# Performance work log

Measured on AMD Instinct MI355X. Metric: run time of the kernel, lower is better.

## Reference

```python
import jax, jax.numpy as jnp
import numpy as np

SHIFT = 1  # fixed instance of the random +/-1 shift_direction


def setup_inputs() -> dict:
    key = jax.random.key(0)
    k1, k2 = jax.random.split(key)
    x = jax.random.normal(k1, (128, 256, 28, 28), dtype=jnp.float32)
    W = jax.random.normal(k2, (128, 3, 128), dtype=jnp.float32)  # (j=in, k=3, i=out)
    return {"x": x, "W": W}


def reference(x, W):
    B, G, Cg, H, Wd = 128, 2, 128, 28, 28
    # view as (l, o, j, n, m) = (batch, group, chan, h, w)
    xg = x.reshape(B, G, Cg, H, Wd)
    # circular roll along width (original: roll(t, shift, dim=4))
    xg = jnp.roll(xg, SHIFT, axis=4)
    # unfold(3,1) pad (1,0) + einsum 'lojnmk, jki -> lonmi' is exactly a
    # zero-padded 1D conv along width with full channel mixing, shared over
    # group and h. Express it as a single grouped-batch conv.
    xm = xg.reshape(B * G, Cg, H, Wd)                 # (N, C, H, W)
    kern = jnp.transpose(W, (2, 0, 1))[:, :, None, :]  # (i, j, 1, 3) OIHW
    y = jax.lax.conv_general_dilated(
        xm, kern, window_strides=(1, 1), padding=((0, 0), (1, 1)),
        dimension_numbers=("NCHW", "OIHW", "NCHW"))   # (B*G, i, H, W)
    y = y.reshape(B, G, Cg, H, Wd)                    # (l, o, i, n, m)
    # second roll is along h (dim 1 of the (l,n,m,o*i) layout == n here)
    y = jnp.roll(y, SHIFT, axis=3)
    # final layout (l, o*i, n, m) == (128, 256, 28, 28)
    return y.reshape(B, G * Cg, H, Wd)
```

## Files before the change

kernel.cpp:

```cpp
#include <hip/hip_runtime.h>


typedef __bf16 bf16x8 __attribute__((ext_vector_type(8)));
typedef float  f32x4  __attribute__((ext_vector_type(4)));

__device__ __forceinline__ int swz(int r, int j) {
    return r * 128 + (j ^ ((r & 7) << 3));
}

#define STAGE_WRITE(BUF, V, J, MQ)                                   \
    {                                                                \
        _Pragma("unroll")                                            \
        for (int e = 0; e < 4; ++e) {                                \
            const int m = (MQ) * 4 + e;                              \
            const int r = (m == 27) ? 1 : (m + 2);                   \
            union { __bf16 h; unsigned short u; } cv;                \
            cv.h = (__bf16)((&(V).x)[e]);                            \
            xsp[BUF][swz(r, (J))] = cv.u;                            \
        }                                                            \
    }

__global__ __launch_bounds__(512, 4)
void shiftconv_kernel(const float* __restrict__ x,
                      const float* __restrict__ Wm,
                      float* __restrict__ out)
{
    __shared__ unsigned short xsp[2][34 * 128];

    const int tid  = threadIdx.x;
    const int wave = tid >> 6;
    const int lane = tid & 63;
    const int l15  = lane & 15;
    const int hi2  = lane >> 4;

    const int b  = blockIdx.x;
    const int l  = b >> 3;
    const int o  = (b >> 2) & 1;
    const int nc = b & 3;

    const float* xbase = x   + (size_t)(l * 256 + o * 128) * 784;
    float*       obase = out + (size_t)(l * 256 + o * 128) * 784;

    const int ga  = tid;
    const int gb  = tid + 512;
    const int ja  = ga / 7,  ma = ga - ja * 7;
    const int jb2 = gb / 7,  mb = gb - jb2 * 7;
    const bool vb = (gb < 896);

    int n1 = nc * 7;

    float4 pa = *reinterpret_cast<const float4*>(xbase + ja * 784 + n1 * 28 + ma * 4);
    float4 pb = make_float4(0.f, 0.f, 0.f, 0.f);
    if (vb) pb = *reinterpret_cast<const float4*>(xbase + jb2 * 784 + n1 * 28 + mb * 4);

    const int ig = wave * 16 + l15;
    bf16x8 bw[12];
#pragma unroll
    for (int s = 0; s < 12; ++s) {
        const int kw = s >> 2;
        const int jb = (s & 3) * 32 + hi2 * 8;
#pragma unroll
        for (int e = 0; e < 8; ++e)
            bw[s][e] = (__bf16)Wm[((jb + e) * 3 + kw) * 128 + ig];
    }

    {
        const int buf = tid >> 8;
        const int r   = ((tid >> 7) & 1) ? 29 : 0;
        const int j   = tid & 127;
        xsp[buf][swz(r, j)] = 0;
    }

    STAGE_WRITE(0, pa, ja, ma);
    if (vb) STAGE_WRITE(0, pb, jb2, mb);

    int cur = 0;
#pragma unroll 1
    for (int t = 0; t < 7; ++t) {
        __syncthreads();

        float4 na, nb;
        const bool more = (t < 6);
        if (more) {
            na = *reinterpret_cast<const float4*>(xbase + ja * 784 + (n1 + 1) * 28 + ma * 4);
            if (vb) nb = *reinterpret_cast<const float4*>(xbase + jb2 * 784 + (n1 + 1) * 28 + mb * 4);
        }

        f32x4 acc0 = {0.f, 0.f, 0.f, 0.f};
        f32x4 acc1 = {0.f, 0.f, 0.f, 0.f};
        const unsigned short* xs = xsp[cur];
#pragma unroll
        for (int s = 0; s < 12; ++s) {
            const int kw = s >> 2;
            const int jb = (s & 3) * 32 + hi2 * 8;
            const bf16x8 a0 = *reinterpret_cast<const bf16x8*>(&xs[swz(l15 + kw, jb)]);
            acc0 = __builtin_amdgcn_mfma_f32_16x16x32_bf16(a0, bw[s], acc0, 0, 0, 0);
            const bf16x8 a1 = *reinterpret_cast<const bf16x8*>(&xs[swz(16 + l15 + kw, jb)]);
            acc1 = __builtin_amdgcn_mfma_f32_16x16x32_bf16(a1, bw[s], acc1, 0, 0, 0);
        }

        const int n = (n1 + 1) % 28;
        float* op = obase + (size_t)ig * 784 + n * 28;
        *reinterpret_cast<float4*>(op + hi2 * 4) =
            make_float4(acc0[0], acc0[1], acc0[2], acc0[3]);
        if (hi2 < 3)
            *reinterpret_cast<float4*>(op + 16 + hi2 * 4) =
                make_float4(acc1[0], acc1[1], acc1[2], acc1[3]);

        if (more) {
            STAGE_WRITE(cur ^ 1, na, ja, ma);
            if (vb) STAGE_WRITE(cur ^ 1, nb, jb2, mb);
        }
        cur ^= 1;
        ++n1;
    }
}

extern "C" void kernel_launch(void* const* d_in, const int* in_sizes, int n_in,
                              void* d_out, int out_size, void* d_ws, size_t ws_size,
                              hipStream_t stream) {
    const float* x  = (const float*)d_in[0];
    const float* Wm = (const float*)d_in[1];
    float* out = (float*)d_out;
    hipLaunchKernelGGL(shiftconv_kernel, dim3(1024), dim3(512), 0, stream, x, Wm, out);
}
```

Before: 222.7 us.

## Split output channels across blocks and prefetch input rows two ahead

Halves the block size to 256 threads and doubles the grid, so each block computes 64 output channels instead of 128. Input rows are now loaded two iterations ahead into register sets, and the loop is fully unrolled with raw s_barrier calls and s_setprio around the MFMA section. The LDS swizzle is also changed to key on row pairs. The cost is that each block stages the full input rows for only half the outputs, so input reads and bf16 conversions are duplicated across the two channel halves.

```diff
diff --git a/kernel.cpp b/kernel.cpp
--- a/kernel.cpp
+++ b/kernel.cpp
@@ -5,22 +5,35 @@
 typedef float  f32x4  __attribute__((ext_vector_type(4)));
 
 __device__ __forceinline__ int swz(int r, int j) {
-    return r * 128 + (j ^ ((r & 7) << 3));
+    return r * 128 + (j ^ (((r >> 1) & 7) << 3));
 }
 
-#define STAGE_WRITE(BUF, V, J, MQ)                                   \
-    {                                                                \
-        _Pragma("unroll")                                            \
-        for (int e = 0; e < 4; ++e) {                                \
-            const int m = (MQ) * 4 + e;                              \
-            const int r = (m == 27) ? 1 : (m + 2);                   \
-            union { __bf16 h; unsigned short u; } cv;                \
-            cv.h = (__bf16)((&(V).x)[e]);                            \
-            xsp[BUF][swz(r, (J))] = cv.u;                            \
-        }                                                            \
+#define LOADROW(SET, T)                                                        \
+    {                                                                          \
+        SET[0] = *reinterpret_cast<const float4*>(cbase[0] + (T) * 28);        \
+        SET[1] = *reinterpret_cast<const float4*>(cbase[1] + (T) * 28);        \
+        SET[2] = *reinterpret_cast<const float4*>(cbase[2] + (T) * 28);        \
+        if (v3) SET[3] = *reinterpret_cast<const float4*>(cbase[3] + (T) * 28);\
     }
 
-__global__ __launch_bounds__(512, 4)
+#define STAGEROW(SET, BUF)                                                     \
+    {                                                                          \
+        _Pragma("unroll")                                                      \
+        for (int c = 0; c < 4; ++c) {                                          \
+            if (c < 3 || v3) {                                                 \
+                _Pragma("unroll")                                              \
+                for (int e = 0; e < 4; ++e) {                                  \
+                    const int m = cm[c] * 4 + e;                               \
+                    const int r = (m == 27) ? 1 : (m + 2);                     \
+                    union { __bf16 h; unsigned short u; } cv;                  \
+                    cv.h = (__bf16)((&SET[c].x)[e]);                           \
+                    xsp[BUF][swz(r, cj[c])] = cv.u;                            \
+                }                                                              \
+            }                                                                  \
+        }                                                                      \
+    }
+
+__global__ __launch_bounds__(256, 4)
 void shiftconv_kernel(const float* __restrict__ x,
                       const float* __restrict__ Wm,
                       float* __restrict__ out)
@@ -34,26 +47,16 @@
     const int hi2  = lane >> 4;
 
     const int b  = blockIdx.x;
-    const int l  = b >> 3;
-    const int o  = (b >> 2) & 1;
+    const int l  = b >> 4;
+    const int o  = (b >> 3) & 1;
+    const int ih = (b >> 2) & 1;
     const int nc = b & 3;
 
-    const float* xbase = x   + (size_t)(l * 256 + o * 128) * 784;
+    const float* xbase = x   + (size_t)(l * 256 + o * 128) * 784 + nc * 7 * 28;
     float*       obase = out + (size_t)(l * 256 + o * 128) * 784;
 
-    const int ga  = tid;
-    const int gb  = tid + 512;
-    const int ja  = ga / 7,  ma = ga - ja * 7;
-    const int jb2 = gb / 7,  mb = gb - jb2 * 7;
-    const bool vb = (gb < 896);
+    const int ig = ih * 64 + wave * 16 + l15;
 
-    int n1 = nc * 7;
-
-    float4 pa = *reinterpret_cast<const float4*>(xbase + ja * 784 + n1 * 28 + ma * 4);
-    float4 pb = make_float4(0.f, 0.f, 0.f, 0.f);
-    if (vb) pb = *reinterpret_cast<const float4*>(xbase + jb2 * 784 + n1 * 28 + mb * 4);
-
-    const int ig = wave * 16 + l15;
     bf16x8 bw[12];
 #pragma unroll
     for (int s = 0; s < 12; ++s) {
@@ -64,31 +67,48 @@
             bw[s][e] = (__bf16)Wm[((jb + e) * 3 + kw) * 128 + ig];
     }
 
-    {
-        const int buf = tid >> 8;
-        const int r   = ((tid >> 7) & 1) ? 29 : 0;
-        const int j   = tid & 127;
-        xsp[buf][swz(r, j)] = 0;
+    int cj[4], cm[4];
+    const float* cbase[4];
+#pragma unroll
+    for (int c = 0; c < 4; ++c) {
+        const int g = tid + 256 * c;
+        const int j = g / 7;
+        cj[c] = j;
+        cm[c] = g - j * 7;
+        cbase[c] = xbase + j * 784 + cm[c] * 4;
+    }
+    const bool v3 = (tid < 128);
+
+#pragma unroll
+    for (int k = 0; k < 2; ++k) {
+        const int idx = tid + 256 * k;
+        const int bu  = idx >> 8;
+        const int r   = (idx & 128) ? 29 : 0;
+        const int j   = idx & 127;
+        xsp[bu][swz(r, j)] = 0;
     }
 
-    STAGE_WRITE(0, pa, ja, ma);
-    if (vb) STAGE_WRITE(0, pb, jb2, mb);
+    float4 ra[4], rb[4];
+    LOADROW(ra, 0);
+    LOADROW(rb, 1);
+    STAGEROW(ra, 0);
+    asm volatile("s_waitcnt lgkmcnt(0)" ::: "memory");
+    __builtin_amdgcn_sched_barrier(0);
+    __builtin_amdgcn_s_barrier();
+    __builtin_amdgcn_sched_barrier(0);
 
-    int cur = 0;
-#pragma unroll 1
+#pragma unroll
     for (int t = 0; t < 7; ++t) {
-        __syncthreads();
+        const int cur = t & 1;
 
-        float4 na, nb;
-        const bool more = (t < 6);
-        if (more) {
-            na = *reinterpret_cast<const float4*>(xbase + ja * 784 + (n1 + 1) * 28 + ma * 4);
-            if (vb) nb = *reinterpret_cast<const float4*>(xbase + jb2 * 784 + (n1 + 1) * 28 + mb * 4);
+        if (t + 2 < 7) {
+            if (cur == 0) { LOADROW(ra, t + 2) } else { LOADROW(rb, t + 2) }
         }
 
         f32x4 acc0 = {0.f, 0.f, 0.f, 0.f};
         f32x4 acc1 = {0.f, 0.f, 0.f, 0.f};
         const unsigned short* xs = xsp[cur];
+        __builtin_amdgcn_s_setprio(1);
 #pragma unroll
         for (int s = 0; s < 12; ++s) {
             const int kw = s >> 2;
@@ -98,8 +118,10 @@
             const bf16x8 a1 = *reinterpret_cast<const bf16x8*>(&xs[swz(16 + l15 + kw, jb)]);
             acc1 = __builtin_amdgcn_mfma_f32_16x16x32_bf16(a1, bw[s], acc1, 0, 0, 0);
         }
+        __builtin_amdgcn_s_setprio(0);
 
-        const int n = (n1 + 1) % 28;
+        const int n1 = nc * 7 + t;
+        int n = n1 + 1; if (n == 28) n = 0;
         float* op = obase + (size_t)ig * 784 + n * 28;
         *reinterpret_cast<float4*>(op + hi2 * 4) =
             make_float4(acc0[0], acc0[1], acc0[2], acc0[3]);
@@ -107,12 +129,13 @@
             *reinterpret_cast<float4*>(op + 16 + hi2 * 4) =
                 make_float4(acc1[0], acc1[1], acc1[2], acc1[3]);
 
-        if (more) {
-            STAGE_WRITE(cur ^ 1, na, ja, ma);
-            if (vb) STAGE_WRITE(cur ^ 1, nb, jb2, mb);
+        if (t + 1 < 7) {
+            if (cur == 0) { STAGEROW(rb, 1) } else { STAGEROW(ra, 0) }
+            asm volatile("s_waitcnt lgkmcnt(0)" ::: "memory");
+            __builtin_amdgcn_sched_barrier(0);
+            __builtin_amdgcn_s_barrier();
+            __builtin_amdgcn_sched_barrier(0);
         }
-        cur ^= 1;
-        ++n1;
     }
 }
 
@@ -122,5 +145,5 @@
     const float* x  = (const float*)d_in[0];
     const float* Wm = (const float*)d_in[1];
     float* out = (float*)d_out;
-    hipLaunchKernelGGL(shiftconv_kernel, dim3(1024), dim3(512), 0, stream, x, Wm, out);
+    hipLaunchKernelGGL(shiftconv_kernel, dim3(2048), dim3(256), 0, stream, x, Wm, out);
 }
```

Measured after the change: 384.0 us. 1.72x slower.

## Preload all seven rows into LDS with one sync and transpose MFMA output

Applied to the files above, without the earlier changes.

Replaces the double-buffered per-row pipeline with a single up-front load of all seven input rows into a larger LDS tile, followed by one barrier. The MFMA operands are swapped so each lane writes scalar outputs contiguous along width, and the LDS swizzle is changed. The aim is more loads in flight and fewer barriers. The cost is much higher register pressure (13 float4 staged per thread) and about 60KB of LDS per block, which may lower occupancy or cause spills under the launch bounds.

```diff
diff --git a/kernel.cpp b/kernel.cpp
--- a/kernel.cpp
+++ b/kernel.cpp
@@ -4,28 +4,16 @@
 typedef __bf16 bf16x8 __attribute__((ext_vector_type(8)));
 typedef float  f32x4  __attribute__((ext_vector_type(4)));
 
-__device__ __forceinline__ int swz(int r, int j) {
-    return r * 128 + (j ^ ((r & 7) << 3));
+__device__ __forceinline__ int swz(int t, int r, int j) {
+    return (t * 34 + r) * 128 + (j ^ (((r >> 1) & 7) << 3));
 }
-
-#define STAGE_WRITE(BUF, V, J, MQ)                                   \
-    {                                                                \
-        _Pragma("unroll")                                            \
-        for (int e = 0; e < 4; ++e) {                                \
-            const int m = (MQ) * 4 + e;                              \
-            const int r = (m == 27) ? 1 : (m + 2);                   \
-            union { __bf16 h; unsigned short u; } cv;                \
-            cv.h = (__bf16)((&(V).x)[e]);                            \
-            xsp[BUF][swz(r, (J))] = cv.u;                            \
-        }                                                            \
-    }
 
 __global__ __launch_bounds__(512, 4)
 void shiftconv_kernel(const float* __restrict__ x,
                       const float* __restrict__ Wm,
                       float* __restrict__ out)
 {
-    __shared__ unsigned short xsp[2][34 * 128];
+    __shared__ unsigned short xs[7 * 34 * 128];
 
     const int tid  = threadIdx.x;
     const int wave = tid >> 6;
@@ -38,20 +26,23 @@
     const int o  = (b >> 2) & 1;
     const int nc = b & 3;
 
-    const float* xbase = x   + (size_t)(l * 256 + o * 128) * 784;
+    const float* xbase = x   + (size_t)(l * 256 + o * 128) * 784 + nc * 7 * 28;
     float*       obase = out + (size_t)(l * 256 + o * 128) * 784;
 
-    const int ga  = tid;
-    const int gb  = tid + 512;
-    const int ja  = ga / 7,  ma = ga - ja * 7;
-    const int jb2 = gb / 7,  mb = gb - jb2 * 7;
-    const bool vb = (gb < 896);
-
-    int n1 = nc * 7;
-
-    float4 pa = *reinterpret_cast<const float4*>(xbase + ja * 784 + n1 * 28 + ma * 4);
-    float4 pb = make_float4(0.f, 0.f, 0.f, 0.f);
-    if (vb) pb = *reinterpret_cast<const float4*>(xbase + jb2 * 784 + n1 * 28 + mb * 4);
+    float4 v[13];
+    int toff[13], joff[13], moff[13];
+#pragma unroll
+    for (int c = 0; c < 13; ++c) {
+        if (c < 12 || tid < 128) {
+            const int g   = tid + 512 * c;
+            const int t   = g / 896;
+            const int rem = g - t * 896;
+            const int j   = rem / 7;
+            const int mq  = rem - j * 7;
+            toff[c] = t; joff[c] = j; moff[c] = mq;
+            v[c] = *reinterpret_cast<const float4*>(xbase + j * 784 + t * 28 + mq * 4);
+        }
+    }
 
     const int ig = wave * 16 + l15;
     bf16x8 bw[12];
@@ -64,55 +55,54 @@
             bw[s][e] = (__bf16)Wm[((jb + e) * 3 + kw) * 128 + ig];
     }
 
-    {
-        const int buf = tid >> 8;
-        const int r   = ((tid >> 7) & 1) ? 29 : 0;
-        const int j   = tid & 127;
-        xsp[buf][swz(r, j)] = 0;
+#pragma unroll
+    for (int k = 0; k < 4; ++k) {
+        const int idx = tid + 512 * k;
+        if (idx < 1792) {
+            const int t = idx >> 8;
+            const int r = (idx & 128) ? 29 : 0;
+            const int j = idx & 127;
+            xs[swz(t, r, j)] = 0;
+        }
     }
 
-    STAGE_WRITE(0, pa, ja, ma);
-    if (vb) STAGE_WRITE(0, pb, jb2, mb);
+#pragma unroll
+    for (int c = 0; c < 13; ++c) {
+        if (c < 12 || tid < 128) {
+#pragma unroll
+            for (int e = 0; e < 4; ++e) {
+                const int m = moff[c] * 4 + e;
+                const int r = (m == 27) ? 1 : (m + 2);
+                union { __bf16 h; unsigned short u; } cv;
+                cv.h = (__bf16)((&v[c].x)[e]);
+                xs[swz(toff[c], r, joff[c])] = cv.u;
+            }
+        }
+    }
 
-    int cur = 0;
-#pragma unroll 1
+    __syncthreads();
+
+#pragma unroll
     for (int t = 0; t < 7; ++t) {
-        __syncthreads();
-
-        float4 na, nb;
-        const bool more = (t < 6);
-        if (more) {
-            na = *reinterpret_cast<const float4*>(xbase + ja * 784 + (n1 + 1) * 28 + ma * 4);
-            if (vb) nb = *reinterpret_cast<const float4*>(xbase + jb2 * 784 + (n1 + 1) * 28 + mb * 4);
-        }
-
         f32x4 acc0 = {0.f, 0.f, 0.f, 0.f};
         f32x4 acc1 = {0.f, 0.f, 0.f, 0.f};
-        const unsigned short* xs = xsp[cur];
 #pragma unroll
         for (int s = 0; s < 12; ++s) {
             const int kw = s >> 2;
             const int jb = (s & 3) * 32 + hi2 * 8;
-            const bf16x8 a0 = *reinterpret_cast<const bf16x8*>(&xs[swz(l15 + kw, jb)]);
-            acc0 = __builtin_amdgcn_mfma_f32_16x16x32_bf16(a0, bw[s], acc0, 0, 0, 0);
-            const bf16x8 a1 = *reinterpret_cast<const bf16x8*>(&xs[swz(16 + l15 + kw, jb)]);
-            acc1 = __builtin_amdgcn_mfma_f32_16x16x32_bf16(a1, bw[s], acc1, 0, 0, 0);
+            const bf16x8 a0 = *reinterpret_cast<const bf16x8*>(&xs[swz(t, l15 + kw, jb)]);
+            acc0 = __builtin_amdgcn_mfma_f32_16x16x32_bf16(bw[s], a0, acc0, 0, 0, 0);
+            const bf16x8 a1 = *reinterpret_cast<const bf16x8*>(&xs[swz(t, 16 + l15 + kw, jb)]);
+            acc1 = __builtin_amdgcn_mfma_f32_16x16x32_bf16(bw[s], a1, acc1, 0, 0, 0);
         }
 
-        const int n = (n1 + 1) % 28;
-        float* op = obase + (size_t)ig * 784 + n * 28;
-        *reinterpret_cast<float4*>(op + hi2 * 4) =
-            make_float4(acc0[0], acc0[1], acc0[2], acc0[3]);
-        if (hi2 < 3)
-            *reinterpret_cast<float4*>(op + 16 + hi2 * 4) =
-                make_float4(acc1[0], acc1[1], acc1[2], acc1[3]);
-
-        if (more) {
-            STAGE_WRITE(cur ^ 1, na, ja, ma);
-            if (vb) STAGE_WRITE(cur ^ 1, nb, jb2, mb);
+        const int n = (nc * 7 + t + 1) % 28;
+#pragma unroll
+        for (int e = 0; e < 4; ++e) {
+            float* op = obase + (size_t)(wave * 16 + 4 * hi2 + e) * 784 + n * 28;
+            op[l15] = acc0[e];
+            if (l15 < 12) op[16 + l15] = acc1[e];
         }
-        cur ^= 1;
-        ++n1;
     }
 }
 
```

Result: slower. 285.9 us (+28.4%).
